# Optimization experiments

Hardware: AMD Instinct MI355X
Metric: run time of the kernel (lower is better)

## Reference

```python
import jax, jax.numpy as jnp
import numpy as np

B, MBS, F, CD = 512, 32768, 512, 16  # batch, mini_batch_size, filter_length, cond_dim

def setup_inputs() -> dict:
    key = jax.random.key(0)
    ks = jax.random.split(key, 8)
    return {
        "inputs": jax.random.normal(ks[0], (B, MBS, 1), jnp.float32),
        "c": jax.random.normal(ks[1], (B, 1, CD), jnp.float32),
        "W0": jax.random.normal(ks[2], (CD, F), jnp.float32) * 0.1,
        "b0": jnp.zeros((F,), jnp.float32),
        "alpha": jnp.full((F,), 0.25, jnp.float32),
        "Wg": jax.random.normal(ks[3], (CD, F), jnp.float32) * 0.1,
        "bg": jnp.zeros((F,), jnp.float32),
        "Wb": jax.random.normal(ks[4], (CD, F), jnp.float32) * 0.1,
        "bb": jnp.zeros((F,), jnp.float32),
        "Wglu": jax.random.normal(ks[5], (F, 2 * F), jnp.float32) * 0.05,
        "bglu": jnp.zeros((2 * F,), jnp.float32),
        "Wf": jax.random.normal(ks[6], (F, F), jnp.float32) * 0.05,
        "bf": jnp.zeros((F,), jnp.float32),
    }

def reference(inputs, c, W0, b0, alpha, Wg, bg, Wb, bb, Wglu, bglu, Wf, bf):
    mbs = inputs.shape[1]
    flen = Wf.shape[1]
    # conditioning stack: Dense -> PReLU -> FiLM -> GLU -> Dense(softsign)
    c_ = c @ W0 + b0                                  # [B,1,F]
    c_ = jnp.where(c_ >= 0, c_, alpha * c_)           # PReLU
    c_ = c_ * (c @ Wg + bg) + (c @ Wb + bb)           # FiLM
    g = c_ @ Wglu + bglu                              # [B,1,2F]
    a, gate = jnp.split(g, 2, axis=-1)
    c_ = a * jax.nn.sigmoid(gate)                     # GLU
    filters = jax.nn.soft_sign(c_ @ Wf + bf)          # [B,1,F]
    # FFT-based circular (linear via zero pad) convolution
    conv_len = mbs + flen - 1
    X = jnp.fft.fft(inputs[:, :, 0].astype(jnp.complex64), n=conv_len)   # [B,conv_len]
    H = jnp.fft.fft(filters[:, 0, :].astype(jnp.complex64), n=conv_len)  # [B,conv_len]
    y = jnp.fft.ifft(X * H)
    return jnp.real(y[:, :mbs])                       # [B,MBS]
```

## Files before the change

### kernel.cpp

```cpp
#include <hip/hip_runtime.h>


typedef float f32x16 __attribute__((ext_vector_type(16)));
typedef float f32x4  __attribute__((ext_vector_type(4)));
typedef __bf16 bf16x8 __attribute__((ext_vector_type(8)));

__device__ __forceinline__ unsigned short f2bf(float f) {
    unsigned int u = __float_as_uint(f);
    u += 0x7FFFu + ((u >> 16) & 1u);
    return (unsigned short)(u >> 16);
}

__global__ __launch_bounds__(256) void kA(
    const float* __restrict__ Wglu, const float* __restrict__ Wf,
    const float* __restrict__ c, const float* __restrict__ W0,
    const float* __restrict__ b0, const float* __restrict__ alpha,
    const float* __restrict__ Wg, const float* __restrict__ bg,
    const float* __restrict__ Wb, const float* __restrict__ bb,
    unsigned short* __restrict__ WgluT, unsigned short* __restrict__ WfT,
    unsigned short* __restrict__ cfilm) {
    const int blk = blockIdx.x, tid = threadIdx.x;
    if (blk < 192) {
        __shared__ float ldsF[64 * 65];
        const float* src; unsigned short* dst; int tj, tk, srcld;
        if (blk < 128) { tj = blk >> 3; tk = blk & 7; src = Wglu; dst = WgluT; srcld = 1024; }
        else { int b2 = blk - 128; tj = b2 >> 3; tk = b2 & 7; src = Wf; dst = WfT; srcld = 512; }
#pragma unroll
        for (int rr = 0; rr < 16; ++rr) {
            int kl = (tid >> 6) + (rr << 2), jl = tid & 63;
            ldsF[kl * 65 + jl] = src[(size_t)(tk * 64 + kl) * srcld + tj * 64 + jl];
        }
        __syncthreads();
#pragma unroll
        for (int rr = 0; rr < 16; ++rr) {
            int jl = (tid >> 6) + (rr << 2), kl = tid & 63;
            dst[(size_t)(tj * 64 + jl) * 512 + tk * 64 + kl] = f2bf(ldsF[kl * 65 + jl]);
        }
    } else {
        int id = (blk - 192) * 256 + tid;
        int b = id >> 9, f = id & 511;
        const float* cb = c + b * 16;
        float d0 = 0.f, dg = 0.f, db = 0.f;
#pragma unroll
        for (int i = 0; i < 16; ++i) {
            float cv = cb[i];
            d0 += cv * W0[i * 512 + f];
            dg += cv * Wg[i * 512 + f];
            db += cv * Wb[i * 512 + f];
        }
        float pre = d0 + b0[f];
        float pr = pre >= 0.f ? pre : alpha[f] * pre;
        float v = pr * (dg + bg[f]) + (db + bb[f]);
        cfilm[id] = f2bf(v);
    }
}

__global__ __launch_bounds__(256) void k2_glu(
    const unsigned short* __restrict__ cfilm, const unsigned short* __restrict__ WgluT,
    const float* __restrict__ bglu, unsigned short* __restrict__ cglu) {
    int wid = (blockIdx.x * 256 + threadIdx.x) >> 6;
    int l = threadIdx.x & 63;
    int tm = wid >> 5, tn = wid & 31;
    int row = tm * 16 + (l & 15);
    int col = tn * 16 + (l & 15);
    int kh = 8 * (l >> 4);
    f32x4 accA, accG;
#pragma unroll
    for (int i = 0; i < 4; ++i) { accA[i] = 0.f; accG[i] = 0.f; }
    const unsigned short* ap  = cfilm + row * 512 + kh;
    const unsigned short* bap = WgluT + col * 512 + kh;
    const unsigned short* bgp = WgluT + (512 + col) * 512 + kh;
#pragma unroll
    for (int kc = 0; kc < 16; ++kc) {
        bf16x8 a   = *(const bf16x8*)(ap  + kc * 32);
        bf16x8 ba  = *(const bf16x8*)(bap + kc * 32);
        bf16x8 bgt = *(const bf16x8*)(bgp + kc * 32);
        accA = __builtin_amdgcn_mfma_f32_16x16x32_bf16(a, ba,  accA, 0, 0, 0);
        accG = __builtin_amdgcn_mfma_f32_16x16x32_bf16(a, bgt, accG, 0, 0, 0);
    }
    float biasA = bglu[col], biasG = bglu[512 + col];
#pragma unroll
    for (int r = 0; r < 4; ++r) {
        float ga = accA[r] + biasA;
        float gg = accG[r] + biasG;
        float s = 1.f / (1.f + expf(-gg));
        int m = (l >> 4) * 4 + r;
        cglu[(tm * 16 + m) * 512 + col] = f2bf(ga * s);
    }
}

__global__ __launch_bounds__(256) void k3_filt(
    const unsigned short* __restrict__ cglu, const unsigned short* __restrict__ WfT,
    const float* __restrict__ bfv, unsigned short* __restrict__ hout) {
    int wid = (blockIdx.x * 256 + threadIdx.x) >> 6;
    int l = threadIdx.x & 63;
    int tm = wid >> 5, tn = wid & 31;
    int row = tm * 16 + (l & 15);
    int col = tn * 16 + (l & 15);
    int kh = 8 * (l >> 4);
    f32x4 acc;
#pragma unroll
    for (int i = 0; i < 4; ++i) acc[i] = 0.f;
    const unsigned short* ap = cglu + row * 512 + kh;
    const unsigned short* bp = WfT + col * 512 + kh;
#pragma unroll
    for (int kc = 0; kc < 16; ++kc) {
        bf16x8 a  = *(const bf16x8*)(ap + kc * 32);
        bf16x8 bv = *(const bf16x8*)(bp + kc * 32);
        acc = __builtin_amdgcn_mfma_f32_16x16x32_bf16(a, bv, acc, 0, 0, 0);
    }
    float bias = bfv[col];
#pragma unroll
    for (int r = 0; r < 4; ++r) {
        float z = acc[r] + bias;
        float h = z / (1.f + fabsf(z));
        int m = (l >> 4) * 4 + r;
        hout[(tm * 16 + m) * 512 + col] = f2bf(h);
    }
}

__global__ __launch_bounds__(512, 4) void k4n(
    const float* __restrict__ x, const unsigned short* __restrict__ hbf,
    float* __restrict__ y) {
    __shared__ __align__(16) unsigned char smem[69632];
    const int tid = threadIdx.x;
    const int b = blockIdx.x >> 1;
    const int n0 = (blockIdx.x & 1) << 14;

    unsigned short* hs = (unsigned short*)(smem + 33792);
    if (tid < 256)
        ((unsigned int*)hs)[tid] = ((const unsigned int*)(hbf + (size_t)b * 512))[tid];

    const float* xb = x + (size_t)b * 32768;
#pragma unroll
    for (int it = 0; it < 5; ++it) {
        int u = tid + (it << 9);
        if (u < 2112) {
            int g0 = n0 - 512 + (u << 3);
            unsigned short us[8];
            if (g0 >= 0) {
                const float4* p = (const float4*)(xb + g0);
                float4 v0 = p[0], v1 = p[1];
                us[0] = f2bf(v0.x); us[1] = f2bf(v0.y); us[2] = f2bf(v0.z); us[3] = f2bf(v0.w);
                us[4] = f2bf(v1.x); us[5] = f2bf(v1.y); us[6] = f2bf(v1.z); us[7] = f2bf(v1.w);
            } else {
#pragma unroll
                for (int i = 0; i < 8; ++i) us[i] = 0;
            }
            int su = u ^ ((u >> 3) & 7);
            unsigned int q0 = us[0] | ((unsigned int)us[1] << 16);
            unsigned int q1 = us[2] | ((unsigned int)us[3] << 16);
            unsigned int q2 = us[4] | ((unsigned int)us[5] << 16);
            unsigned int q3 = us[6] | ((unsigned int)us[7] << 16);
            *(uint4*)(smem + (su << 4)) = make_uint4(q0, q1, q2, q3);
        }
    }
    __syncthreads();

    unsigned short* Bb = (unsigned short*)(smem + 34816);
    for (int e = tid; e < 34 * 64; e += 512) {
        int cc = e >> 6, ll = e & 63;
        int base = 16 * cc - 16 + (ll & 31) - 8 * (ll >> 5);
        unsigned short vals[8];
#pragma unroll
        for (int i = 0; i < 8; ++i) {
            int idx = base - i;
            vals[i] = (idx >= 0 && idx < 512) ? hs[idx] : (unsigned short)0;
        }
        unsigned int q0 = vals[0] | ((unsigned int)vals[1] << 16);
        unsigned int q1 = vals[2] | ((unsigned int)vals[3] << 16);
        unsigned int q2 = vals[4] | ((unsigned int)vals[5] << 16);
        unsigned int q3 = vals[6] | ((unsigned int)vals[7] << 16);
        *(uint4*)(Bb + e * 8) = make_uint4(q0, q1, q2, q3);
    }
    __syncthreads();

    const int w = tid >> 6, l = tid & 63;
    const int lq = 4 * (l & 31) + (l >> 5);
    const int ubase = (w << 8) + 66 + lq;
    f32x16 acc0, acc1;
#pragma unroll
    for (int i = 0; i < 16; ++i) { acc0[i] = 0.f; acc1[i] = 0.f; }
    const unsigned char* Bp = smem + 34816 + l * 16;
    for (int cc = 0; cc < 34; ++cc) {
        bf16x8 bfr = *(const bf16x8*)(Bp + cc * 1024);
        int u0 = ubase - 2 * cc;
        int u1 = u0 + 128;
        const bf16x8 a0 = *(const bf16x8*)(smem + ((u0 ^ ((u0 >> 3) & 7)) << 4));
        const bf16x8 a1 = *(const bf16x8*)(smem + ((u1 ^ ((u1 >> 3) & 7)) << 4));
        acc0 = __builtin_amdgcn_mfma_f32_32x32x16_bf16(a0, bfr, acc0, 0, 0, 0);
        acc1 = __builtin_amdgcn_mfma_f32_32x32x16_bf16(a1, bfr, acc1, 0, 0, 0);
    }
    float* yb = y + (size_t)b * 32768 + n0 + (w << 11) + (l & 31);
#pragma unroll
    for (int r = 0; r < 16; ++r) {
        int m = (r & 3) + 8 * (r >> 2) + 4 * (l >> 5);
        yb[m << 5] = acc0[r];
        yb[1024 + (m << 5)] = acc1[r];
    }
}

extern "C" void kernel_launch(void* const* d_in, const int* in_sizes, int n_in,
                              void* d_out, int out_size, void* d_ws, size_t ws_size,
                              hipStream_t stream) {
    const float* x    = (const float*)d_in[0];
    const float* c    = (const float*)d_in[1];
    const float* W0   = (const float*)d_in[2];
    const float* b0   = (const float*)d_in[3];
    const float* al   = (const float*)d_in[4];
    const float* Wg   = (const float*)d_in[5];
    const float* bg   = (const float*)d_in[6];
    const float* Wb   = (const float*)d_in[7];
    const float* bb   = (const float*)d_in[8];
    const float* Wglu = (const float*)d_in[9];
    const float* bglu = (const float*)d_in[10];
    const float* Wf   = (const float*)d_in[11];
    const float* bf   = (const float*)d_in[12];
    float* y = (float*)d_out;

    char* ws = (char*)d_ws;
    unsigned short* cfilm = (unsigned short*)(ws);
    unsigned short* WgluT = (unsigned short*)(ws + 524288);
    unsigned short* WfT   = (unsigned short*)(ws + 1572864);
    unsigned short* cglu  = (unsigned short*)(ws + 2097152);
    unsigned short* hbf   = (unsigned short*)(ws + 2621440);

    kA<<<dim3(1216), dim3(256), 0, stream>>>(Wglu, Wf, c, W0, b0, al, Wg, bg, Wb, bb,
                                             WgluT, WfT, cfilm);
    k2_glu<<<dim3(256), dim3(256), 0, stream>>>(cfilm, WgluT, bglu, cglu);
    k3_filt<<<dim3(256), dim3(256), 0, stream>>>(cglu, WfT, bf, hbf);
    k4n<<<dim3(1024), dim3(512), 0, stream>>>(x, hbf, y);
}
```

Measured before the change: 53.00 us.

## Restructure conv kernel into per-batch block with double-buffered x chunks

Replaces the two-blocks-per-batch Toeplitz MFMA convolution with one 256-thread block per batch row. The block walks four 8192-sample chunks, prefetching the next chunk into registers during the first half of the MFMA loop and writing it to a second LDS buffer. The filter Toeplitz fragment table is built as a compact shifted-pair layout instead of a 34x64x8 expansion, and float-to-bf16 packing uses native conversions. The aim is to hide global loads behind compute and to cut setup cost, in exchange for fewer blocks, lower occupancy and more register pressure.

```diff
diff --git a/kernel.cpp b/kernel.cpp
--- a/kernel.cpp
+++ b/kernel.cpp
@@ -9,6 +9,15 @@
     unsigned int u = __float_as_uint(f);
     u += 0x7FFFu + ((u >> 16) & 1u);
     return (unsigned short)(u >> 16);
+}
+
+__device__ __forceinline__ uint4 pack8n(float4 a, float4 b) {
+    bf16x8 v;
+    v[0] = (__bf16)a.x; v[1] = (__bf16)a.y; v[2] = (__bf16)a.z; v[3] = (__bf16)a.w;
+    v[4] = (__bf16)b.x; v[5] = (__bf16)b.y; v[6] = (__bf16)b.z; v[7] = (__bf16)b.w;
+    uint4 r;
+    __builtin_memcpy(&r, &v, 16);
+    return r;
 }
 
 __global__ __launch_bounds__(256) void kA(
@@ -119,84 +128,112 @@
     }
 }
 
-__global__ __launch_bounds__(512, 4) void k4n(
+__global__ __launch_bounds__(256, 2) void k5(
     const float* __restrict__ x, const unsigned short* __restrict__ hbf,
     float* __restrict__ y) {
-    __shared__ __align__(16) unsigned char smem[69632];
+    __shared__ __align__(16) unsigned char smem[45184];
     const int tid = threadIdx.x;
-    const int b = blockIdx.x >> 1;
-    const int n0 = (blockIdx.x & 1) << 14;
-
-    unsigned short* hs = (unsigned short*)(smem + 33792);
-    if (tid < 256)
-        ((unsigned int*)hs)[tid] = ((const unsigned int*)(hbf + (size_t)b * 512))[tid];
-
+    const int b = blockIdx.x;
     const float* xb = x + (size_t)b * 32768;
-#pragma unroll
-    for (int it = 0; it < 5; ++it) {
-        int u = tid + (it << 9);
-        if (u < 2112) {
-            int g0 = n0 - 512 + (u << 3);
-            unsigned short us[8];
-            if (g0 >= 0) {
-                const float4* p = (const float4*)(xb + g0);
-                float4 v0 = p[0], v1 = p[1];
-                us[0] = f2bf(v0.x); us[1] = f2bf(v0.y); us[2] = f2bf(v0.z); us[3] = f2bf(v0.w);
-                us[4] = f2bf(v1.x); us[5] = f2bf(v1.y); us[6] = f2bf(v1.z); us[7] = f2bf(v1.w);
+    unsigned short* hs = (unsigned short*)(smem + 44160);
+
+    ((unsigned int*)hs)[tid] = ((const unsigned int*)(hbf + (size_t)b * 512))[tid];
+    __syncthreads();
+
+    for (int e = tid; e < 8 * 292; e += 256) {
+        int s = e / 292, w = e - s * 292;
+        int j0 = 2 * w + s;
+        unsigned int v0 = (j0 >= 32 && j0 < 544) ? hs[543 - j0] : 0u;
+        unsigned int v1 = (j0 >= 31 && j0 < 543) ? hs[542 - j0] : 0u;
+        ((unsigned int*)(smem + 34816))[e] = v0 | (v1 << 16);
+    }
+
+#pragma unroll
+    for (int r = 0; r < 5; ++r) {
+        int slot = tid + (r << 8);
+        if (slot < 1088) {
+            int g = slot - 64;
+            uint4 w4;
+            if (g >= 0) {
+                float4 a  = *(const float4*)(xb + g * 8);
+                float4 b2 = *(const float4*)(xb + g * 8 + 4);
+                w4 = pack8n(a, b2);
             } else {
-#pragma unroll
-                for (int i = 0; i < 8; ++i) us[i] = 0;
+                w4 = make_uint4(0u, 0u, 0u, 0u);
             }
-            int su = u ^ ((u >> 3) & 7);
-            unsigned int q0 = us[0] | ((unsigned int)us[1] << 16);
-            unsigned int q1 = us[2] | ((unsigned int)us[3] << 16);
-            unsigned int q2 = us[4] | ((unsigned int)us[5] << 16);
-            unsigned int q3 = us[6] | ((unsigned int)us[7] << 16);
-            *(uint4*)(smem + (su << 4)) = make_uint4(q0, q1, q2, q3);
+            *(uint4*)(smem + ((slot ^ ((slot >> 3) & 7)) << 4)) = w4;
         }
     }
     __syncthreads();
 
-    unsigned short* Bb = (unsigned short*)(smem + 34816);
-    for (int e = tid; e < 34 * 64; e += 512) {
-        int cc = e >> 6, ll = e & 63;
-        int base = 16 * cc - 16 + (ll & 31) - 8 * (ll >> 5);
-        unsigned short vals[8];
-#pragma unroll
-        for (int i = 0; i < 8; ++i) {
-            int idx = base - i;
-            vals[i] = (idx >= 0 && idx < 512) ? hs[idx] : (unsigned short)0;
-        }
-        unsigned int q0 = vals[0] | ((unsigned int)vals[1] << 16);
-        unsigned int q1 = vals[2] | ((unsigned int)vals[3] << 16);
-        unsigned int q2 = vals[4] | ((unsigned int)vals[5] << 16);
-        unsigned int q3 = vals[6] | ((unsigned int)vals[7] << 16);
-        *(uint4*)(Bb + e * 8) = make_uint4(q0, q1, q2, q3);
-    }
-    __syncthreads();
-
     const int w = tid >> 6, l = tid & 63;
-    const int lq = 4 * (l & 31) + (l >> 5);
-    const int ubase = (w << 8) + 66 + lq;
-    f32x16 acc0, acc1;
-#pragma unroll
-    for (int i = 0; i < 16; ++i) { acc0[i] = 0.f; acc1[i] = 0.f; }
-    const unsigned char* Bp = smem + 34816 + l * 16;
-    for (int cc = 0; cc < 34; ++cc) {
-        bf16x8 bfr = *(const bf16x8*)(Bp + cc * 1024);
-        int u0 = ubase - 2 * cc;
-        int u1 = u0 + 128;
-        const bf16x8 a0 = *(const bf16x8*)(smem + ((u0 ^ ((u0 >> 3) & 7)) << 4));
-        const bf16x8 a1 = *(const bf16x8*)(smem + ((u1 ^ ((u1 >> 3) & 7)) << 4));
-        acc0 = __builtin_amdgcn_mfma_f32_32x32x16_bf16(a0, bfr, acc0, 0, 0, 0);
-        acc1 = __builtin_amdgcn_mfma_f32_32x32x16_bf16(a1, bfr, acc1, 0, 0, 0);
-    }
-    float* yb = y + (size_t)b * 32768 + n0 + (w << 11) + (l & 31);
-#pragma unroll
-    for (int r = 0; r < 16; ++r) {
-        int m = (r & 3) + 8 * (r >> 2) + 4 * (l >> 5);
-        yb[m << 5] = acc0[r];
-        yb[1024 + (m << 5)] = acc1[r];
+    const int q = l & 31, hl = l >> 5;
+    const int lq = 4 * q + hl;
+    const int abase = 66 + (w << 8) + lq;
+    const int o0 = 559 - q + 8 * hl;
+    const int s8 = o0 & 7;
+    const unsigned char* hrb = smem + 34816 + s8 * 1168 + ((o0 - s8) << 1);
+
+    for (int c = 0; c < 4; ++c) {
+        const unsigned char* wb = smem + ((c & 1) ? 17408 : 0);
+        unsigned char* sb = smem + ((c & 1) ? 0 : 17408);
+        float4 La0, La1, La2, La3, La4, Lb0, Lb1, Lb2, Lb3, Lb4;
+        if (c < 3) {
+            const float* px = xb + (((c + 1) << 13) - 512);
+            La0 = *(const float4*)(px + (tid << 3));           Lb0 = *(const float4*)(px + (tid << 3) + 4);
+            La1 = *(const float4*)(px + ((tid + 256) << 3));   Lb1 = *(const float4*)(px + ((tid + 256) << 3) + 4);
+            La2 = *(const float4*)(px + ((tid + 512) << 3));   Lb2 = *(const float4*)(px + ((tid + 512) << 3) + 4);
+            La3 = *(const float4*)(px + ((tid + 768) << 3));   Lb3 = *(const float4*)(px + ((tid + 768) << 3) + 4);
+            if (tid < 64) {
+                La4 = *(const float4*)(px + ((tid + 1024) << 3));
+                Lb4 = *(const float4*)(px + ((tid + 1024) << 3) + 4);
+            }
+        }
+        f32x16 acc0, acc1;
+#pragma unroll
+        for (int i = 0; i < 16; ++i) { acc0[i] = 0.f; acc1[i] = 0.f; }
+#pragma unroll
+        for (int cc = 0; cc < 17; ++cc) {
+            bf16x8 bfr = *(const bf16x8*)(hrb - (cc << 5));
+            int a0 = abase - 2 * cc, a1 = a0 + 128;
+            bf16x8 xa0 = *(const bf16x8*)(wb + ((a0 ^ ((a0 >> 3) & 7)) << 4));
+            bf16x8 xa1 = *(const bf16x8*)(wb + ((a1 ^ ((a1 >> 3) & 7)) << 4));
+            acc0 = __builtin_amdgcn_mfma_f32_32x32x16_bf16(xa0, bfr, acc0, 0, 0, 0);
+            acc1 = __builtin_amdgcn_mfma_f32_32x32x16_bf16(xa1, bfr, acc1, 0, 0, 0);
+        }
+        if (c < 3) {
+            int s0 = tid;
+            *(uint4*)(sb + ((s0 ^ ((s0 >> 3) & 7)) << 4)) = pack8n(La0, Lb0);
+            int s1 = tid + 256;
+            *(uint4*)(sb + ((s1 ^ ((s1 >> 3) & 7)) << 4)) = pack8n(La1, Lb1);
+            int s2 = tid + 512;
+            *(uint4*)(sb + ((s2 ^ ((s2 >> 3) & 7)) << 4)) = pack8n(La2, Lb2);
+            int s3 = tid + 768;
+            *(uint4*)(sb + ((s3 ^ ((s3 >> 3) & 7)) << 4)) = pack8n(La3, Lb3);
+            if (tid < 64) {
+                int s4 = tid + 1024;
+                *(uint4*)(sb + ((s4 ^ ((s4 >> 3) & 7)) << 4)) = pack8n(La4, Lb4);
+            }
+        }
+#pragma unroll
+        for (int cc = 17; cc < 34; ++cc) {
+            bf16x8 bfr = *(const bf16x8*)(hrb - (cc << 5));
+            int a0 = abase - 2 * cc, a1 = a0 + 128;
+            bf16x8 xa0 = *(const bf16x8*)(wb + ((a0 ^ ((a0 >> 3) & 7)) << 4));
+            bf16x8 xa1 = *(const bf16x8*)(wb + ((a1 ^ ((a1 >> 3) & 7)) << 4));
+            acc0 = __builtin_amdgcn_mfma_f32_32x32x16_bf16(xa0, bfr, acc0, 0, 0, 0);
+            acc1 = __builtin_amdgcn_mfma_f32_32x32x16_bf16(xa1, bfr, acc1, 0, 0, 0);
+        }
+        asm volatile("s_waitcnt lgkmcnt(0)" ::: "memory");
+        __builtin_amdgcn_s_barrier();
+        __builtin_amdgcn_sched_barrier(0);
+        float* yb = y + (size_t)b * 32768 + (c << 13) + (w << 11) + q;
+#pragma unroll
+        for (int r = 0; r < 16; ++r) {
+            int m = (r & 3) + 8 * (r >> 2) + 4 * hl;
+            yb[m << 5] = acc0[r];
+            yb[1024 + (m << 5)] = acc1[r];
+        }
     }
 }
 
@@ -229,5 +266,5 @@
                                              WgluT, WfT, cfilm);
     k2_glu<<<dim3(256), dim3(256), 0, stream>>>(cfilm, WgluT, bglu, cglu);
     k3_filt<<<dim3(256), dim3(256), 0, stream>>>(cglu, WfT, bf, hbf);
-    k4n<<<dim3(1024), dim3(512), 0, stream>>>(x, hbf, y);
-}
+    k5<<<dim3(512), dim3(256), 0, stream>>>(x, hbf, y);
+}
```

New measurement: 49.55 us. -6.5%, faster.
